# Optimization experiments

Hardware: AMD Instinct MI355X
Metric: run time of the kernel (lower is better)

Reference implementation:

```python
import jax, jax.numpy as jnp
import numpy as np

N_NODES = 100000
N_EDGES = 1600000
N_FEAT = 64
HIDDEN = 64
N_GRAPHS = 128


def gcn_conv(x, edge_index, W, b, n_nodes):
    # PyG GCNConv defaults: x @ W (no bias), add self-loops, sym-normalize,
    # scatter-add aggregate, then add bias.
    src, dst = edge_index[0], edge_index[1]
    loops = jnp.arange(n_nodes, dtype=src.dtype)
    src = jnp.concatenate([src, loops])
    dst = jnp.concatenate([dst, loops])
    deg = jax.ops.segment_sum(jnp.ones_like(src, dtype=x.dtype), dst,
                              num_segments=n_nodes)
    dinv = jnp.where(deg > 0, jax.lax.rsqrt(jnp.maximum(deg, 1e-12)), 0.0)
    norm = dinv[src] * dinv[dst]                      # [E+N]
    xw = x @ W                                        # [N, H]
    msg = xw[src] * norm[:, None]                     # gather + scale [E+N, H]
    out = jax.ops.segment_sum(msg, dst, num_segments=n_nodes)  # scatter-add
    return out + b


def setup_inputs() -> dict:
    key = jax.random.key(0)
    ks = jax.random.split(key, 12)
    x = jax.random.normal(ks[0], (N_NODES, N_FEAT), dtype=jnp.float32)
    edge_index = jax.random.randint(ks[1], (2, N_EDGES), 0, N_NODES, dtype=jnp.int64)
    batch = jnp.sort(jax.random.randint(ks[2], (N_NODES,), 0, N_GRAPHS, dtype=jnp.int64))
    s = 0.05
    W1 = jax.random.normal(ks[3], (N_FEAT, HIDDEN), dtype=jnp.float32) * s
    b1 = jnp.zeros((HIDDEN,), dtype=jnp.float32)
    W2 = jax.random.normal(ks[4], (HIDDEN, HIDDEN), dtype=jnp.float32) * s
    b2 = jnp.zeros((HIDDEN,), dtype=jnp.float32)
    fc1_w = jax.random.normal(ks[5], (HIDDEN, HIDDEN), dtype=jnp.float32) * s
    fc1_b = jnp.zeros((HIDDEN,), dtype=jnp.float32)
    fc2_w = jax.random.normal(ks[6], (HIDDEN, 1), dtype=jnp.float32) * s
    fc2_b = jnp.zeros((1,), dtype=jnp.float32)
    return {"x": x, "edge_index": edge_index, "batch": batch,
            "W1": W1, "b1": b1, "W2": W2, "b2": b2,
            "fc1_w": fc1_w, "fc1_b": fc1_b, "fc2_w": fc2_w, "fc2_b": fc2_b}


def reference(x, edge_index, batch, W1, b1, W2, b2, fc1_w, fc1_b, fc2_w, fc2_b):
    n = x.shape[0]
    h = jax.nn.relu(gcn_conv(x, edge_index, W1, b1, n))
    h = jax.nn.relu(gcn_conv(h, edge_index, W2, b2, n))
    g = jax.ops.segment_sum(h, batch, num_segments=N_GRAPHS)  # global_add_pool
    g = jax.nn.relu(g @ fc1_w + fc1_b)
    return g @ fc2_w + fc2_b  # [N_GRAPHS, 1]
```

## Files before the change

kernel.cpp:

```cpp
#include <hip/hip_runtime.h>
#include <hip/hip_fp16.h>


#define NODES_PER_GEMM_BLOCK 16
#define BSHIFT 9
#define NBK_MAX 256
#define EPT 16

union HU2 { uint2 u; __half2 h[2]; };
union HU4 { uint4 u; __half2 h[4]; };

__device__ __forceinline__ void st_h4(__half* __restrict__ y, int node, int c, float4 v) {
    HU2 p;
    p.h[0] = __floats2half2_rn(v.x, v.y);
    p.h[1] = __floats2half2_rn(v.z, v.w);
    *(uint2*)(y + ((size_t)node << 6) + c) = p.u;
}

__device__ __forceinline__ void accum8(float* a, const HU4& p, float m) {
#pragma unroll
    for (int q = 0; q < 4; ++q) {
        float2 f = __half22float2(p.h[q]);
        a[2 * q]     = fmaf(f.x, m, a[2 * q]);
        a[2 * q + 1] = fmaf(f.y, m, a[2 * q + 1]);
    }
}

__device__ __forceinline__ void gather_row8(float* acc, const __half* __restrict__ y,
                                            const int* __restrict__ col,
                                            int node, int c8, int beg, int end) {
    HU4 self;
    self.u = *(const uint4*)(y + ((size_t)node << 6) + c8);
    accum8(acc, self, 1.0f);
    int lim = end - 1;
    for (int j = beg; j < end; j += 8) {
        HU4 v[8];
#pragma unroll
        for (int u = 0; u < 8; ++u) {
            int p = (j + u <= lim) ? j + u : lim;
            v[u].u = *(const uint4*)(y + ((size_t)col[p] << 6) + c8);
        }
#pragma unroll
        for (int u = 0; u < 8; ++u)
            accum8(acc, v[u], (j + u <= lim) ? 1.0f : 0.0f);
    }
}

__global__ void k_zero_int(int* __restrict__ p, int n) {
    int i = blockIdx.x * blockDim.x + threadIdx.x;
    if (i < n) p[i] = 0;
}

__global__ void k_bhist(const int* __restrict__ dst, int* __restrict__ bcnt,
                        int E, int nbk) {
    __shared__ int c[NBK_MAX];
    int t = threadIdx.x;
    for (int i = t; i < nbk; i += 256) c[i] = 0;
    __syncthreads();
    for (int e = blockIdx.x * blockDim.x + t; e < E; e += gridDim.x * blockDim.x)
        atomicAdd(&c[dst[e] >> BSHIFT], 1);
    __syncthreads();
    for (int i = t; i < nbk; i += 256)
        if (c[i]) atomicAdd(&bcnt[i], c[i]);
}

__global__ void k_bscan(const int* __restrict__ bcnt, int* __restrict__ bbase,
                        int* __restrict__ bcursor, int* __restrict__ row_ptr,
                        int nbk, int n, int E) {
    __shared__ int s[NBK_MAX];
    int t = threadIdx.x;
    int v0 = (t < nbk) ? bcnt[t] : 0;
    s[t] = v0;
    __syncthreads();
    for (int o = 1; o < 256; o <<= 1) {
        int v = (t >= o) ? s[t - o] : 0;
        __syncthreads();
        s[t] += v;
        __syncthreads();
    }
    int exc = s[t] - v0;
    if (t < nbk) { bbase[t] = exc; bcursor[t] = exc; }
    if (t == 0) { bbase[nbk] = E; row_ptr[n] = E; }
}

__global__ void k_binpairs(const int* __restrict__ src, const int* __restrict__ dst,
                           int* __restrict__ bcursor, int2* __restrict__ ebuf,
                           int E, int nbk) {
    __shared__ int cnt[NBK_MAX], base[NBK_MAX];
    int t = threadIdx.x;
    for (int i = t; i < nbk; i += 256) cnt[i] = 0;
    __syncthreads();
    int e0 = blockIdx.x * (256 * EPT);
    int d[EPT], s[EPT];
#pragma unroll
    for (int j = 0; j < EPT; ++j) {
        int e = e0 + j * 256 + t;
        if (e < E) {
            d[j] = dst[e]; s[j] = src[e];
            atomicAdd(&cnt[d[j] >> BSHIFT], 1);
        } else d[j] = -1;
    }
    __syncthreads();
    for (int i = t; i < nbk; i += 256)
        base[i] = cnt[i] ? atomicAdd(&bcursor[i], cnt[i]) : 0;
    __syncthreads();
    for (int i = t; i < nbk; i += 256) cnt[i] = 0;
    __syncthreads();
#pragma unroll
    for (int j = 0; j < EPT; ++j) {
        if (d[j] >= 0) {
            int b = d[j] >> BSHIFT;
            int r = atomicAdd(&cnt[b], 1);
            ebuf[base[b] + r] = make_int2(d[j], s[j]);
        }
    }
}

__global__ void k_bucket_csr(const int2* __restrict__ ebuf, const int* __restrict__ bbase,
                             int* __restrict__ row_ptr, int* __restrict__ col,
                             float* __restrict__ dinv, int n) {
    __shared__ int cnt[512], ofs[512], cur[512];
    __shared__ int ssum[256];
    int b = blockIdx.x;
    int t = threadIdx.x;
    int nodeBase = b << BSHIFT;
    int nNodes = min(512, n - nodeBase);
    int beg = bbase[b], end = bbase[b + 1];
    cnt[t] = 0; cnt[t + 256] = 0;
    __syncthreads();
    for (int e = beg + t; e < end; e += 256)
        atomicAdd(&cnt[ebuf[e].x - nodeBase], 1);
    __syncthreads();
    int a0 = cnt[2 * t], a1 = cnt[2 * t + 1];
    ssum[t] = a0 + a1;
    __syncthreads();
    for (int o = 1; o < 256; o <<= 1) {
        int v = (t >= o) ? ssum[t - o] : 0;
        __syncthreads();
        ssum[t] += v;
        __syncthreads();
    }
    int exc = ssum[t] - (a0 + a1);
    ofs[2 * t] = exc;       ofs[2 * t + 1] = exc + a0;
    cur[2 * t] = exc;       cur[2 * t + 1] = exc + a0;
    __syncthreads();
    for (int i = t; i < nNodes; i += 256) {
        row_ptr[nodeBase + i] = beg + ofs[i];
        dinv[nodeBase + i] = rsqrtf((float)(cnt[i] + 1));
    }
    __syncthreads();
    for (int e = beg + t; e < end; e += 256) {
        int2 p = ebuf[e];
        int r = atomicAdd(&cur[p.x - nodeBase], 1);
        col[beg + r] = p.y;
    }
}

__global__ void k_gemm64(const float* __restrict__ in, const float* __restrict__ W,
                         const float* __restrict__ dinv, __half* __restrict__ out, int n) {
    __shared__ float Ws[64 * 64];
    int t = threadIdx.x;
#pragma unroll
    for (int j = 0; j < 4; ++j) {
        int idx = (t + j * 256) * 4;
        *(float4*)&Ws[idx] = *(const float4*)&W[idx];
    }
    __syncthreads();
    int row = blockIdx.x * NODES_PER_GEMM_BLOCK + (t >> 4);
    int c = (t & 15) * 4;
    if (row >= n) return;
    const float* inr = in + (size_t)row * 64;
    float4 acc = make_float4(0.f, 0.f, 0.f, 0.f);
#pragma unroll
    for (int k0 = 0; k0 < 64; k0 += 4) {
        float4 xv = *(const float4*)(inr + k0);
        float xs[4] = {xv.x, xv.y, xv.z, xv.w};
#pragma unroll
        for (int j = 0; j < 4; ++j) {
            float4 w = *(const float4*)&Ws[(k0 + j) * 64 + c];
            acc.x += xs[j] * w.x; acc.y += xs[j] * w.y;
            acc.z += xs[j] * w.z; acc.w += xs[j] * w.w;
        }
    }
    float s = dinv[row];
    acc.x *= s; acc.y *= s; acc.z *= s; acc.w *= s;
    st_h4(out, row, c, acc);
}

__global__ void k_gather_gemm(const __half* __restrict__ y, const int* __restrict__ row_ptr,
                              const int* __restrict__ col, const float* __restrict__ dinv,
                              const float* __restrict__ bias, const float* __restrict__ W,
                              __half* __restrict__ out, int n) {
    __shared__ float Ws[64 * 64];
    __shared__ float rowb[32][72];
    int t = threadIdx.x;
#pragma unroll
    for (int j = 0; j < 4; ++j) {
        int idx = (t + j * 256) * 4;
        *(float4*)&Ws[idx] = *(const float4*)&W[idx];
    }
    int nl = t >> 3;
    int node = blockIdx.x * 32 + nl;
    int c8 = (t & 7) * 8;
    bool active = node < n;
    float dn = 0.f;
    if (active) {
        float acc[8] = {0.f, 0.f, 0.f, 0.f, 0.f, 0.f, 0.f, 0.f};
        int beg = row_ptr[node], end = row_ptr[node + 1];
        gather_row8(acc, y, col, node, c8, beg, end);
        dn = dinv[node];
#pragma unroll
        for (int f = 0; f < 8; ++f)
            rowb[nl][c8 + f] = fmaxf(fmaf(acc[f], dn, bias[c8 + f]), 0.f);
    }
    __syncthreads();
    if (!active) return;
    float o[8] = {0.f, 0.f, 0.f, 0.f, 0.f, 0.f, 0.f, 0.f};
#pragma unroll 8
    for (int k = 0; k < 64; ++k) {
        float xk = rowb[nl][k];
        const float* wr = &Ws[k * 64 + c8];
#pragma unroll
        for (int f = 0; f < 8; ++f) o[f] = fmaf(xk, wr[f], o[f]);
    }
    HU4 p;
#pragma unroll
    for (int q = 0; q < 4; ++q)
        p.h[q] = __floats2half2_rn(o[2 * q] * dn, o[2 * q + 1] * dn);
    *(uint4*)(out + ((size_t)node << 6) + c8) = p.u;
}

__global__ void k_gather_pool(const __half* __restrict__ y, const int* __restrict__ row_ptr,
                              const int* __restrict__ col, const float* __restrict__ dinv,
                              const float* __restrict__ bias, const int* __restrict__ batch,
                              float* __restrict__ g, int n) {
    int t = threadIdx.x;
    int blk0 = (int)blockIdx.x * 32;
    int nl = t >> 3;
    int node = blk0 + nl;
    int c8 = (t & 7) * 8;
    __shared__ int bFirst, bLast;
    __shared__ float gl[4 * 64];
    if (t == 0) {
        int i0 = blk0 < n - 1 ? blk0 : n - 1;
        bFirst = batch[i0];
    }
    if (t == 255) {
        int i1 = blk0 + 31 < n - 1 ? blk0 + 31 : n - 1;
        bLast = batch[i1];
    }
    bool active = node < n;
    float h[8] = {0.f, 0.f, 0.f, 0.f, 0.f, 0.f, 0.f, 0.f};
    int bt = 0;
    if (active) {
        float acc[8] = {0.f, 0.f, 0.f, 0.f, 0.f, 0.f, 0.f, 0.f};
        int beg = row_ptr[node], end = row_ptr[node + 1];
        gather_row8(acc, y, col, node, c8, beg, end);
        float dn = dinv[node];
#pragma unroll
        for (int f = 0; f < 8; ++f)
            h[f] = fmaxf(fmaf(acc[f], dn, bias[c8 + f]), 0.f);
        bt = batch[node];
    }
    __syncthreads();
    if (bFirst == bLast) {
#pragma unroll
        for (int f = 0; f < 8; ++f) {
            h[f] += __shfl_xor(h[f], 8, 64);
            h[f] += __shfl_xor(h[f], 16, 64);
            h[f] += __shfl_xor(h[f], 32, 64);
        }
        int wv = t >> 6;
        if ((t & 63) < 8) {
#pragma unroll
            for (int f = 0; f < 8; ++f) gl[wv * 64 + (t & 7) * 8 + f] = h[f];
        }
        __syncthreads();
        if (t < 64) {
            float tot = gl[t] + gl[64 + t] + gl[128 + t] + gl[192 + t];
            unsafeAtomicAdd(&g[(size_t)bFirst * 64 + t], tot);
        }
    } else if (active) {
        float* gp = &g[(size_t)bt * 64 + c8];
#pragma unroll
        for (int f = 0; f < 8; ++f) unsafeAtomicAdd(gp + f, h[f]);
    }
}

__global__ void k_head(const float* __restrict__ g, const float* __restrict__ fc1w,
                       const float* __restrict__ fc1b, const float* __restrict__ fc2w,
                       const float* __restrict__ fc2b, float* __restrict__ out) {
    int b = blockIdx.x, t = threadIdx.x;
    __shared__ float gl[64];
    gl[t] = g[(size_t)b * 64 + t];
    __syncthreads();
    float acc = fc1b[t];
#pragma unroll 8
    for (int k = 0; k < 64; ++k) acc += gl[k] * fc1w[k * 64 + t];
    float v = fmaxf(acc, 0.f) * fc2w[t];
#pragma unroll
    for (int o = 32; o > 0; o >>= 1) v += __shfl_down(v, o, 64);
    if (t == 0) out[b] = v + fc2b[0];
}

extern "C" void kernel_launch(void* const* d_in, const int* in_sizes, int n_in,
                              void* d_out, int out_size, void* d_ws, size_t ws_size,
                              hipStream_t stream) {
    const float* x    = (const float*)d_in[0];
    const int*   ei   = (const int*)d_in[1];
    const int*   batch= (const int*)d_in[2];
    const float* W1   = (const float*)d_in[3];
    const float* b1   = (const float*)d_in[4];
    const float* W2   = (const float*)d_in[5];
    const float* b2   = (const float*)d_in[6];
    const float* fc1w = (const float*)d_in[7];
    const float* fc1b = (const float*)d_in[8];
    const float* fc2w = (const float*)d_in[9];
    const float* fc2b = (const float*)d_in[10];
    float* out = (float*)d_out;

    int N = in_sizes[0] / 64;
    int E = in_sizes[1] / 2;
    const int* src = ei;
    const int* dstp = ei + E;
    int G = out_size;
    int nbk = (N + (1 << BSHIFT) - 1) >> BSHIFT;

    float*  base    = (float*)d_ws;
    __half* y1      = (__half*)base;
    float*  scratch = base + (size_t)N * 32;
    int2*   ebuf    = (int2*)scratch;
    __half* y2      = (__half*)scratch;
    size_t  scr_w   = (size_t)(N * 32 > E * 2 ? N * 32 : E * 2);
    float*  dinv    = scratch + scr_w;
    int*    row_ptr = (int*)(dinv + N);
    int*    col     = row_ptr + (N + 1);
    int*    bbase   = col + E;
    int*    bcursor = bbase + (NBK_MAX + 1);
    int*    bcnt    = bcursor + NBK_MAX;
    float*  g       = (float*)(bcnt + NBK_MAX);

    dim3 blk(256);
    int nzero = NBK_MAX + G * 64;
    int nb_pairs = (E + 256 * EPT - 1) / (256 * EPT);
    int nb_gemm  = (N + NODES_PER_GEMM_BLOCK - 1) / NODES_PER_GEMM_BLOCK;
    int nb_g32   = (N + 31) / 32;

    k_zero_int<<<(nzero + 255) / 256, blk, 0, stream>>>(bcnt, nzero);
    k_bhist<<<1024, blk, 0, stream>>>(dstp, bcnt, E, nbk);
    k_bscan<<<1, blk, 0, stream>>>(bcnt, bbase, bcursor, row_ptr, nbk, N, E);
    k_binpairs<<<nb_pairs, blk, 0, stream>>>(src, dstp, bcursor, ebuf, E, nbk);
    k_bucket_csr<<<nbk, blk, 0, stream>>>(ebuf, bbase, row_ptr, col, dinv, N);

    k_gemm64<<<nb_gemm, blk, 0, stream>>>(x, W1, dinv, y1, N);
    k_gather_gemm<<<nb_g32, blk, 0, stream>>>(y1, row_ptr, col, dinv, b1, W2, y2, N);
    k_gather_pool<<<nb_g32, blk, 0, stream>>>(y2, row_ptr, col, dinv, b2, batch, g, N);
    k_head<<<G, 64, 0, stream>>>(g, fc1w, fc1b, fc2w, fc2b, out);
}
```

Before: 208.7 us.

## Shrink gather blocks to 128 threads, store W2 as half in LDS, predicate tail loads

The gather kernels move from 32 nodes per 256-thread block to 16 nodes per 128-thread block. k_gather_gemm now keeps W2 in LDS as half2 (8 KB instead of 16 KB) to cut shared-memory use and raise occupancy. The neighbour-gather tail is handled with predicated loads that skip out-of-range edges instead of clamped redundant loads plus multiply-by-zero masking. The pool kernel drops its cross-wave LDS reduction and has each wave issue its own atomics, which doubles the atomic traffic per graph. Rounding W2 to half adds precision error to the second layer.

```diff
diff --git a/kernel.cpp b/kernel.cpp
--- a/kernel.cpp
+++ b/kernel.cpp
@@ -17,12 +17,12 @@
     *(uint2*)(y + ((size_t)node << 6) + c) = p.u;
 }
 
-__device__ __forceinline__ void accum8(float* a, const HU4& p, float m) {
+__device__ __forceinline__ void accum8(float* a, const HU4& p) {
 #pragma unroll
     for (int q = 0; q < 4; ++q) {
         float2 f = __half22float2(p.h[q]);
-        a[2 * q]     = fmaf(f.x, m, a[2 * q]);
-        a[2 * q + 1] = fmaf(f.y, m, a[2 * q + 1]);
+        a[2 * q]     += f.x;
+        a[2 * q + 1] += f.y;
     }
 }
 
@@ -31,18 +31,17 @@
                                             int node, int c8, int beg, int end) {
     HU4 self;
     self.u = *(const uint4*)(y + ((size_t)node << 6) + c8);
-    accum8(acc, self, 1.0f);
-    int lim = end - 1;
+    accum8(acc, self);
     for (int j = beg; j < end; j += 8) {
         HU4 v[8];
 #pragma unroll
         for (int u = 0; u < 8; ++u) {
-            int p = (j + u <= lim) ? j + u : lim;
-            v[u].u = *(const uint4*)(y + ((size_t)col[p] << 6) + c8);
-        }
-#pragma unroll
-        for (int u = 0; u < 8; ++u)
-            accum8(acc, v[u], (j + u <= lim) ? 1.0f : 0.0f);
+            v[u].u = make_uint4(0u, 0u, 0u, 0u);
+            if (j + u < end)
+                v[u].u = *(const uint4*)(y + ((size_t)col[j + u] << 6) + c8);
+        }
+#pragma unroll
+        for (int u = 0; u < 8; ++u) accum8(acc, v[u]);
     }
 }
 
@@ -191,16 +190,15 @@
                               const int* __restrict__ col, const float* __restrict__ dinv,
                               const float* __restrict__ bias, const float* __restrict__ W,
                               __half* __restrict__ out, int n) {
-    __shared__ float Ws[64 * 64];
-    __shared__ float rowb[32][72];
-    int t = threadIdx.x;
-#pragma unroll
-    for (int j = 0; j < 4; ++j) {
-        int idx = (t + j * 256) * 4;
-        *(float4*)&Ws[idx] = *(const float4*)&W[idx];
+    __shared__ __half2 Wh[64 * 32];
+    __shared__ float rowb[16][72];
+    int t = threadIdx.x;
+    for (int i = t; i < 2048; i += 128) {
+        float2 wf = *(const float2*)&W[i * 2];
+        Wh[i] = __floats2half2_rn(wf.x, wf.y);
     }
     int nl = t >> 3;
-    int node = blockIdx.x * 32 + nl;
+    int node = (int)blockIdx.x * 16 + nl;
     int c8 = (t & 7) * 8;
     bool active = node < n;
     float dn = 0.f;
@@ -219,9 +217,13 @@
 #pragma unroll 8
     for (int k = 0; k < 64; ++k) {
         float xk = rowb[nl][k];
-        const float* wr = &Ws[k * 64 + c8];
-#pragma unroll
-        for (int f = 0; f < 8; ++f) o[f] = fmaf(xk, wr[f], o[f]);
+        const __half2* wr = &Wh[k * 32 + (c8 >> 1)];
+#pragma unroll
+        for (int q = 0; q < 4; ++q) {
+            float2 wf = __half22float2(wr[q]);
+            o[2 * q]     = fmaf(xk, wf.x, o[2 * q]);
+            o[2 * q + 1] = fmaf(xk, wf.y, o[2 * q + 1]);
+        }
     }
     HU4 p;
 #pragma unroll
@@ -235,18 +237,17 @@
                               const float* __restrict__ bias, const int* __restrict__ batch,
                               float* __restrict__ g, int n) {
     int t = threadIdx.x;
-    int blk0 = (int)blockIdx.x * 32;
+    int blk0 = (int)blockIdx.x * 16;
     int nl = t >> 3;
     int node = blk0 + nl;
     int c8 = (t & 7) * 8;
     __shared__ int bFirst, bLast;
-    __shared__ float gl[4 * 64];
     if (t == 0) {
         int i0 = blk0 < n - 1 ? blk0 : n - 1;
         bFirst = batch[i0];
     }
-    if (t == 255) {
-        int i1 = blk0 + 31 < n - 1 ? blk0 + 31 : n - 1;
+    if (t == 127) {
+        int i1 = blk0 + 15 < n - 1 ? blk0 + 15 : n - 1;
         bLast = batch[i1];
     }
     bool active = node < n;
@@ -270,15 +271,10 @@
             h[f] += __shfl_xor(h[f], 16, 64);
             h[f] += __shfl_xor(h[f], 32, 64);
         }
-        int wv = t >> 6;
         if ((t & 63) < 8) {
-#pragma unroll
-            for (int f = 0; f < 8; ++f) gl[wv * 64 + (t & 7) * 8 + f] = h[f];
-        }
-        __syncthreads();
-        if (t < 64) {
-            float tot = gl[t] + gl[64 + t] + gl[128 + t] + gl[192 + t];
-            unsafeAtomicAdd(&g[(size_t)bFirst * 64 + t], tot);
+            float* gp = &g[(size_t)bFirst * 64 + c8];
+#pragma unroll
+            for (int f = 0; f < 8; ++f) unsafeAtomicAdd(gp + f, h[f]);
         }
     } else if (active) {
         float* gp = &g[(size_t)bt * 64 + c8];
@@ -344,7 +340,7 @@
     int nzero = NBK_MAX + G * 64;
     int nb_pairs = (E + 256 * EPT - 1) / (256 * EPT);
     int nb_gemm  = (N + NODES_PER_GEMM_BLOCK - 1) / NODES_PER_GEMM_BLOCK;
-    int nb_g32   = (N + 31) / 32;
+    int nb_g16   = (N + 15) / 16;
 
     k_zero_int<<<(nzero + 255) / 256, blk, 0, stream>>>(bcnt, nzero);
     k_bhist<<<1024, blk, 0, stream>>>(dstp, bcnt, E, nbk);
@@ -353,7 +349,7 @@
     k_bucket_csr<<<nbk, blk, 0, stream>>>(ebuf, bbase, row_ptr, col, dinv, N);
 
     k_gemm64<<<nb_gemm, blk, 0, stream>>>(x, W1, dinv, y1, N);
-    k_gather_gemm<<<nb_g32, blk, 0, stream>>>(y1, row_ptr, col, dinv, b1, W2, y2, N);
-    k_gather_pool<<<nb_g32, blk, 0, stream>>>(y2, row_ptr, col, dinv, b2, batch, g, N);
+    k_gather_gemm<<<nb_g16, 128, 0, stream>>>(y1, row_ptr, col, dinv, b1, W2, y2, N);
+    k_gather_pool<<<nb_g16, 128, 0, stream>>>(y2, row_ptr, col, dinv, b2, batch, g, N);
     k_head<<<G, 64, 0, stream>>>(g, fc1w, fc1b, fc2w, fc2b, out);
 }
```

After: 281.9 us. 1.35x slower.
